# Optimization experiments

Measured on AMD Instinct MI355X. Metric: run time of the kernel, lower is better.

Reference implementation:

```python
import jax, jax.numpy as jnp
import numpy as np

HEADS = 16
DIM_HEAD = 64


def setup_inputs() -> dict:
    key = jax.random.key(0)
    k1, k2, k3, k4, k5 = jax.random.split(key, 5)
    B, S, E = 4, 2048, 1024
    inner = HEADS * DIM_HEAD  # 1024
    return {
        "hidden_states": jax.random.normal(k1, (B, S, E), dtype=jnp.float32),
        "w_q": jax.random.normal(k2, (E, inner), dtype=jnp.float32) * (E ** -0.5),
        "w_k": jax.random.normal(k3, (E, inner), dtype=jnp.float32) * (E ** -0.5),
        "w_v": jax.random.normal(k4, (E, inner), dtype=jnp.float32) * (E ** -0.5),
        "w_o": jax.random.normal(k5, (inner, E), dtype=jnp.float32) * (inner ** -0.5),
    }


def reference(hidden_states, w_q, w_k, w_v, w_o):
    # Self-attention path: context = hidden_states (context arg is None).
    B, S, _ = hidden_states.shape
    dtype = hidden_states.dtype
    scale = DIM_HEAD ** -0.5

    q = (hidden_states @ w_q).reshape(B, S, HEADS, DIM_HEAD)
    k = (hidden_states @ w_k).reshape(B, S, HEADS, DIM_HEAD)
    v = (hidden_states @ w_v).reshape(B, S, HEADS, DIM_HEAD)

    # fp32 softmax as in the original module
    q32 = q.astype(jnp.float32)
    k32 = k.astype(jnp.float32)
    scores = jnp.einsum('btnh,bfnh->bnft', k32, q32) * scale  # [B, H, S_q, S_kv]
    probs = jax.nn.softmax(scores, axis=-1).astype(dtype)

    out = jnp.einsum('bnft,btnh->bfnh', probs, v)  # [B, S, H, D]
    out = out.reshape(B, S, HEADS * DIM_HEAD)
    return out @ w_o  # [B, S, query_dim]
```

## Files before the change

kernel.cpp:

```cpp
#include <hip/hip_runtime.h>
#include <stdint.h>

typedef __attribute__((ext_vector_type(8))) unsigned short ushort8;
typedef __attribute__((ext_vector_type(8))) __bf16 bf16x8;
typedef __attribute__((ext_vector_type(4))) float f32x4;
typedef __attribute__((ext_vector_type(4))) uint32_t u32x4;

#define TBK 32

__device__ __forceinline__ unsigned short f2bf(float f) {
  union { float f; uint32_t u; } x; x.f = f;
  uint32_t u = x.u;
  uint32_t r = (u + 0x7fffu + ((u >> 16) & 1u)) >> 16;
  return (unsigned short)r;
}

__device__ __forceinline__ uint32_t pack_bf2(float lo, float hi) {
  return (uint32_t)f2bf(lo) | ((uint32_t)f2bf(hi) << 16);
}

__device__ __forceinline__ uint32_t rhu2(float lo, float hi) {
  union { float f; uint32_t u; } a, b; a.f = lo; b.f = hi;
  return __builtin_amdgcn_perm(b.u + 0x8000u, a.u + 0x8000u, 0x07060302u);
}

__device__ __forceinline__ void store_c(unsigned short* p, float v) { *p = f2bf(v); }
__device__ __forceinline__ void store_c(float* p, float v) { *p = v; }

__device__ __forceinline__ void gll16(const unsigned short* g, unsigned short* l) {
  __builtin_amdgcn_global_load_lds((const __attribute__((address_space(1))) void*)g,
                                   (__attribute__((address_space(3))) void*)l,
                                   16, 0, 0);
}

__global__ __launch_bounds__(256) void cvt_f32_bf16(
    const float* __restrict__ x, unsigned short* __restrict__ y, int n4) {
  int i = blockIdx.x * 256 + threadIdx.x;
  if (i >= n4) return;
  float4 v = *(const float4*)(x + (size_t)i * 4);
  uint2 p; p.x = pack_bf2(v.x, v.y); p.y = pack_bf2(v.z, v.w);
  *(uint2*)(y + (size_t)i * 4) = p;
}

__global__ void transpose_w(const float* __restrict__ W,
                            unsigned short* __restrict__ WT) {
  __shared__ unsigned short tile[32][33];
  int c0 = blockIdx.x * 32, r0 = blockIdx.y * 32;
  int x = threadIdx.x, y = threadIdx.y;
#pragma unroll
  for (int i = 0; i < 32; i += 8)
    tile[y + i][x] = f2bf(W[(size_t)(r0 + y + i) * 1024 + c0 + x]);
  __syncthreads();
#pragma unroll
  for (int i = 0; i < 32; i += 8)
    WT[(size_t)(c0 + y + i) * 1024 + r0 + x] = tile[x][y + i];
}

template <typename OutT>
__global__ __launch_bounds__(256) void gemm_bt(
    const unsigned short* A,
    const unsigned short* BT0, const unsigned short* BT1, const unsigned short* BT2,
    OutT* C0, OutT* C1, OutT* C2,
    int M, int N, int K, float sc0) {
  const unsigned short* BT = (blockIdx.z == 0) ? BT0 : (blockIdx.z == 1) ? BT1 : BT2;
  OutT* C = (blockIdx.z == 0) ? C0 : (blockIdx.z == 1) ? C1 : C2;
  const float sc = (blockIdx.z == 0) ? sc0 : 1.0f;

  __shared__ __attribute__((aligned(16))) unsigned short As[128 * TBK];
  __shared__ __attribute__((aligned(16))) unsigned short Bs[128 * TBK];

  const int tid = threadIdx.x;
  const int wave = tid >> 6, lane = tid & 63;
  const int fr = lane & 15, fq = lane >> 4;
  const int bm = blockIdx.x * 128, bn = blockIdx.y * 128;
  const int wm = (wave >> 1) * 64, wn = (wave & 1) * 64;

  f32x4 acc[4][4] = {};

  const int sr = lane >> 2;
  const int sk = (lane & 3) * 8;
  const unsigned short* Ag = A + (size_t)(bm + wave * 32 + sr) * K + sk;
  const unsigned short* Bg = BT + (size_t)(bn + wave * 32 + sr) * K + sk;
  unsigned short* As0 = &As[(wave * 32) * TBK];
  unsigned short* Bs0 = &Bs[(wave * 32) * TBK];

  for (int k0 = 0; k0 < K; k0 += TBK) {
    gll16(Ag + k0, As0);
    gll16(Ag + k0 + 16 * K, As0 + 16 * TBK);
    gll16(Bg + k0, Bs0);
    gll16(Bg + k0 + 16 * K, Bs0 + 16 * TBK);
    asm volatile("s_waitcnt vmcnt(0)" ::: "memory");
    __syncthreads();

    bf16x8 af[4], bfr[4];
#pragma unroll
    for (int mt = 0; mt < 4; mt++)
      af[mt] = *(const bf16x8*)&As[(wm + mt * 16 + fr) * TBK + fq * 8];
#pragma unroll
    for (int nt = 0; nt < 4; nt++)
      bfr[nt] = *(const bf16x8*)&Bs[(wn + nt * 16 + fr) * TBK + fq * 8];
#pragma unroll
    for (int mt = 0; mt < 4; mt++)
#pragma unroll
      for (int nt = 0; nt < 4; nt++)
        acc[mt][nt] = __builtin_amdgcn_mfma_f32_16x16x32_bf16(af[mt], bfr[nt], acc[mt][nt], 0, 0, 0);
    __syncthreads();
  }

#pragma unroll
  for (int mt = 0; mt < 4; mt++)
#pragma unroll
    for (int nt = 0; nt < 4; nt++)
#pragma unroll
      for (int r = 0; r < 4; r++) {
        int row = bm + wm + mt * 16 + fq * 4 + r;
        int col = bn + wn + nt * 16 + fr;
        store_c(&C[(size_t)row * N + col], acc[mt][nt][r] * sc);
      }
}

__global__ __launch_bounds__(256, 4) void attn_kernel(
    const unsigned short* q, const unsigned short* k,
    const unsigned short* v, unsigned short* o) {
  const int S = 2048, E = 1024;
  __shared__ __attribute__((aligned(16))) unsigned short Ksb[2 * 64 * 64];
  __shared__ __attribute__((aligned(16))) unsigned short Vtb[64 * 64];

  const int tid = threadIdx.x;
  const int wave = tid >> 6, lane = tid & 63;
  const int fr = lane & 15, fq = lane >> 4;
  const int q0 = blockIdx.x * 128;
  const int bh = blockIdx.y;
  const int b = bh >> 4, h = bh & 15;
  const size_t base = ((size_t)b * S) * E + (size_t)h * 64;

  bf16x8 aq[2][2];
#pragma unroll
  for (int qg = 0; qg < 2; qg++)
#pragma unroll
    for (int ks = 0; ks < 2; ks++)
      aq[qg][ks] = *(const bf16x8*)&q[base +
          (size_t)(q0 + qg * 64 + wave * 16 + fr) * E + ks * 32 + fq * 8];

  ushort8 ones_u;
#pragma unroll
  for (int j = 0; j < 8; j++) ones_u[j] = 0x3F80;
  bf16x8 onesf = *(bf16x8*)&ones_u;

  f32x4 ot[2][4] = {};
  f32x4 osum[2] = {};

  const int srow = lane >> 3;
  const int scol = (((lane & 7) ^ srow) << 3);
  const unsigned short* Kg = k + base + (size_t)(wave * 16 + srow) * E + scol;

  const int rp = (tid & 31) * 2;
  const int dcv = (tid >> 5) * 8;
  const int u_ = rp & 31;
  const int slot = 32 * (rp >> 5) + 8 * ((u_ & 15) >> 2) + 4 * (u_ >> 4) + (u_ & 3);
  const unsigned short* Vg = v + base + (size_t)rp * E + dcv;

  const int rx = (fr & 7) << 3;

  gll16(Kg, &Ksb[wave * 1024]);
  gll16(Kg + 8 * (size_t)E, &Ksb[wave * 1024 + 512]);

  int cur = 0;
  for (int t = 0; t < 32; t++) {
    const int nxt = cur ^ 4096;

    const size_t toff = (size_t)t * 64 * E;
    u32x4 va = *(const u32x4*)(Vg + toff);
    u32x4 vb = *(const u32x4*)(Vg + toff + E);

    __syncthreads();

#pragma unroll
    for (int w = 0; w < 4; w++) {
      uint32_t lo = __builtin_amdgcn_perm(vb[w], va[w], 0x05040100u);
      uint32_t hi = __builtin_amdgcn_perm(vb[w], va[w], 0x07060302u);
      int d = dcv + 2 * w;
      *(uint32_t*)&Vtb[d * 64 + (slot ^ ((2 * w) << 3))] = lo;
      *(uint32_t*)&Vtb[(d + 1) * 64 + (slot ^ ((2 * w + 1) << 3))] = hi;
    }

    __syncthreads();

    if (t < 31) {
      const size_t poff = (size_t)(t + 1) * 64 * E;
      gll16(Kg + poff, &Ksb[nxt + wave * 1024]);
      gll16(Kg + poff + 8 * (size_t)E, &Ksb[nxt + wave * 1024 + 512]);
    }

    f32x4 st[2][4] = {};
    __builtin_amdgcn_s_setprio(1);
#pragma unroll
    for (int ks = 0; ks < 2; ks++) {
#pragma unroll
      for (int tt = 0; tt < 4; tt++) {
        bf16x8 ak = *(const bf16x8*)&Ksb[cur + (tt * 16 + fr) * 64 +
                                         ((ks * 32 + fq * 8) ^ rx)];
        st[0][tt] = __builtin_amdgcn_mfma_f32_16x16x32_bf16(ak, aq[0][ks], st[0][tt], 0, 0, 0);
        st[1][tt] = __builtin_amdgcn_mfma_f32_16x16x32_bf16(ak, aq[1][ks], st[1][tt], 0, 0, 0);
      }
    }
    __builtin_amdgcn_s_setprio(0);

    uint32_t pk[2][4][2];
#pragma unroll
    for (int qg = 0; qg < 2; qg++)
#pragma unroll
      for (int tt = 0; tt < 4; tt++) {
        float e0 = __builtin_amdgcn_exp2f(st[qg][tt][0]);
        float e1 = __builtin_amdgcn_exp2f(st[qg][tt][1]);
        float e2 = __builtin_amdgcn_exp2f(st[qg][tt][2]);
        float e3 = __builtin_amdgcn_exp2f(st[qg][tt][3]);
        pk[qg][tt][0] = rhu2(e0, e1);
        pk[qg][tt][1] = rhu2(e2, e3);
      }

    __builtin_amdgcn_s_setprio(1);
#pragma unroll
    for (int c = 0; c < 2; c++) {
      bf16x8 bp[2];
#pragma unroll
      for (int qg = 0; qg < 2; qg++) {
        u32x4 bpr;
        bpr[0] = pk[qg][2 * c][0];
        bpr[1] = pk[qg][2 * c][1];
        bpr[2] = pk[qg][2 * c + 1][0];
        bpr[3] = pk[qg][2 * c + 1][1];
        bp[qg] = *(bf16x8*)&bpr;
      }
#pragma unroll
      for (int dt = 0; dt < 4; dt++) {
        bf16x8 av = *(const bf16x8*)&Vtb[(dt * 16 + fr) * 64 +
                                         ((c * 32 + fq * 8) ^ rx)];
        ot[0][dt] = __builtin_amdgcn_mfma_f32_16x16x32_bf16(av, bp[0], ot[0][dt], 0, 0, 0);
        ot[1][dt] = __builtin_amdgcn_mfma_f32_16x16x32_bf16(av, bp[1], ot[1][dt], 0, 0, 0);
      }
      osum[0] = __builtin_amdgcn_mfma_f32_16x16x32_bf16(onesf, bp[0], osum[0], 0, 0, 0);
      osum[1] = __builtin_amdgcn_mfma_f32_16x16x32_bf16(onesf, bp[1], osum[1], 0, 0, 0);
    }
    __builtin_amdgcn_s_setprio(0);

    cur = nxt;
  }

#pragma unroll
  for (int qg = 0; qg < 2; qg++) {
    float inv = 1.0f / osum[qg][0];
    size_t rowbase = base + (size_t)(q0 + qg * 64 + wave * 16 + fr) * E;
#pragma unroll
    for (int dt = 0; dt < 4; dt++) {
      uint32_t w0 = rhu2(ot[qg][dt][0] * inv, ot[qg][dt][1] * inv);
      uint32_t w1 = rhu2(ot[qg][dt][2] * inv, ot[qg][dt][3] * inv);
      *(uint32_t*)&o[rowbase + dt * 16 + fq * 4] = w0;
      *(uint32_t*)&o[rowbase + dt * 16 + fq * 4 + 2] = w1;
    }
  }
}

extern "C" void kernel_launch(void* const* d_in, const int* in_sizes, int n_in,
                              void* d_out, int out_size, void* d_ws, size_t ws_size,
                              hipStream_t stream) {
  const float* hs = (const float*)d_in[0];
  const float* wq = (const float*)d_in[1];
  const float* wk = (const float*)d_in[2];
  const float* wv = (const float*)d_in[3];
  const float* wo = (const float*)d_in[4];
  unsigned short* ws = (unsigned short*)d_ws;

  unsigned short* wqT = ws;
  unsigned short* wkT = ws + 1048576;
  unsigned short* wvT = ws + 2097152;
  unsigned short* woT = wqT;
  unsigned short* qb  = ws + 3145728;
  unsigned short* kb  = qb + 8388608;
  unsigned short* vb  = kb + 8388608;
  unsigned short* ob  = qb;
  unsigned short* hsb = (unsigned short*)d_out;
  float* out = (float*)d_out;

  const int M = 8192, N = 1024, K = 1024;
  const float KSC = 0.125f * 1.44269504088896341f;

  cvt_f32_bf16<<<dim3(M * K / 4 / 256), 256, 0, stream>>>(hs, hsb, M * K / 4);

  dim3 tb(32, 8);
  transpose_w<<<dim3(32, 32), tb, 0, stream>>>(wq, wqT);
  transpose_w<<<dim3(32, 32), tb, 0, stream>>>(wk, wkT);
  transpose_w<<<dim3(32, 32), tb, 0, stream>>>(wv, wvT);

  gemm_bt<unsigned short><<<dim3(M / 128, N / 128, 3), 256, 0, stream>>>(
      hsb, wqT, wkT, wvT, qb, kb, vb, M, N, K, KSC);

  transpose_w<<<dim3(32, 32), tb, 0, stream>>>(wo, woT);

  attn_kernel<<<dim3(2048 / 128, 64), 256, 0, stream>>>(qb, kb, vb, ob);

  gemm_bt<float><<<dim3(M / 128, N / 128, 1), 256, 0, stream>>>(
      ob, woT, woT, woT, out, out, out, M, N, K, 1.0f);
}
```

Before: 279.1 us.

## Double-buffer GEMM with 128x256 tiles, BK=64, XOR-swizzled LDS, fused transposes

Rewrites the projection GEMM to use 512-thread blocks computing 128x256 tiles. K steps are now 64 wide, and the next tile is prefetched into a second LDS buffer with global_load_lds while MFMAs run on the current one. The LDS column chunks are XOR-swizzled so fragment reads avoid bank conflicts. The three weight transposes are also merged into one launch. The goal is to hide global-load latency, halve the barriers per K element and cut launch count, at the price of more LDS (96KB per block) and fewer resident blocks.

```diff
diff --git a/kernel.cpp b/kernel.cpp
--- a/kernel.cpp
+++ b/kernel.cpp
@@ -5,8 +5,6 @@
 typedef __attribute__((ext_vector_type(8))) __bf16 bf16x8;
 typedef __attribute__((ext_vector_type(4))) float f32x4;
 typedef __attribute__((ext_vector_type(4))) uint32_t u32x4;
-
-#define TBK 32
 
 __device__ __forceinline__ unsigned short f2bf(float f) {
   union { float f; uint32_t u; } x; x.f = f;
@@ -42,8 +40,7 @@
   *(uint2*)(y + (size_t)i * 4) = p;
 }
 
-__global__ void transpose_w(const float* __restrict__ W,
-                            unsigned short* __restrict__ WT) {
+__device__ __forceinline__ void transpose_body(const float* W, unsigned short* WT) {
   __shared__ unsigned short tile[32][33];
   int c0 = blockIdx.x * 32, r0 = blockIdx.y * 32;
   int x = threadIdx.x, y = threadIdx.y;
@@ -56,8 +53,21 @@
     WT[(size_t)(c0 + y + i) * 1024 + r0 + x] = tile[x][y + i];
 }
 
+__global__ void transpose_w(const float* __restrict__ W,
+                            unsigned short* __restrict__ WT) {
+  transpose_body(W, WT);
+}
+
+__global__ void transpose_w3(const float* W0, const float* W1, const float* W2,
+                             unsigned short* T0, unsigned short* T1,
+                             unsigned short* T2) {
+  const float* W = (blockIdx.z == 0) ? W0 : (blockIdx.z == 1) ? W1 : W2;
+  unsigned short* WT = (blockIdx.z == 0) ? T0 : (blockIdx.z == 1) ? T1 : T2;
+  transpose_body(W, WT);
+}
+
 template <typename OutT>
-__global__ __launch_bounds__(256) void gemm_bt(
+__global__ __launch_bounds__(512, 2) void gemm2(
     const unsigned short* A,
     const unsigned short* BT0, const unsigned short* BT1, const unsigned short* BT2,
     OutT* C0, OutT* C1, OutT* C2,
@@ -66,55 +76,77 @@
   OutT* C = (blockIdx.z == 0) ? C0 : (blockIdx.z == 1) ? C1 : C2;
   const float sc = (blockIdx.z == 0) ? sc0 : 1.0f;
 
-  __shared__ __attribute__((aligned(16))) unsigned short As[128 * TBK];
-  __shared__ __attribute__((aligned(16))) unsigned short Bs[128 * TBK];
+  __shared__ __attribute__((aligned(16))) unsigned short As[2][128 * 64];
+  __shared__ __attribute__((aligned(16))) unsigned short Bs[2][256 * 64];
 
   const int tid = threadIdx.x;
   const int wave = tid >> 6, lane = tid & 63;
   const int fr = lane & 15, fq = lane >> 4;
-  const int bm = blockIdx.x * 128, bn = blockIdx.y * 128;
-  const int wm = (wave >> 1) * 64, wn = (wave & 1) * 64;
+  const int wm = wave >> 2, wn = wave & 3;
+  const int bm = blockIdx.x * 128, bn = blockIdx.y * 256;
+
+  const int r8 = tid >> 3, c8 = tid & 7;
+  const int s8 = c8 ^ (r8 & 7);
+  const unsigned short* Ag = A + (size_t)(bm + r8) * K + s8 * 8;
+  const unsigned short* Bg = BT + (size_t)(bn + r8) * K + s8 * 8;
 
   f32x4 acc[4][4] = {};
-
-  const int sr = lane >> 2;
-  const int sk = (lane & 3) * 8;
-  const unsigned short* Ag = A + (size_t)(bm + wave * 32 + sr) * K + sk;
-  const unsigned short* Bg = BT + (size_t)(bn + wave * 32 + sr) * K + sk;
-  unsigned short* As0 = &As[(wave * 32) * TBK];
-  unsigned short* Bs0 = &Bs[(wave * 32) * TBK];
-
-  for (int k0 = 0; k0 < K; k0 += TBK) {
-    gll16(Ag + k0, As0);
-    gll16(Ag + k0 + 16 * K, As0 + 16 * TBK);
-    gll16(Bg + k0, Bs0);
-    gll16(Bg + k0 + 16 * K, Bs0 + 16 * TBK);
-    asm volatile("s_waitcnt vmcnt(0)" ::: "memory");
+  const int rx = fr & 7;
+
+  const int NT = K >> 6;
+
+  {
+    gll16(Ag, &As[0][(wave * 8) * 64]);
+    gll16(Ag + 64 * (size_t)K, &As[0][(64 + wave * 8) * 64]);
+    gll16(Bg, &Bs[0][(wave * 8) * 64]);
+    gll16(Bg + 64 * (size_t)K, &Bs[0][(64 + wave * 8) * 64]);
+    gll16(Bg + 128 * (size_t)K, &Bs[0][(128 + wave * 8) * 64]);
+    gll16(Bg + 192 * (size_t)K, &Bs[0][(192 + wave * 8) * 64]);
+  }
+
+  int cur = 0;
+  for (int t = 0; t < NT; ++t) {
     __syncthreads();
 
-    bf16x8 af[4], bfr[4];
-#pragma unroll
-    for (int mt = 0; mt < 4; mt++)
-      af[mt] = *(const bf16x8*)&As[(wm + mt * 16 + fr) * TBK + fq * 8];
+    if (t + 1 < NT) {
+      const int b = cur ^ 1;
+      const size_t k0 = (size_t)(t + 1) * 64;
+      gll16(Ag + k0, &As[b][(wave * 8) * 64]);
+      gll16(Ag + k0 + 64 * (size_t)K, &As[b][(64 + wave * 8) * 64]);
+      gll16(Bg + k0, &Bs[b][(wave * 8) * 64]);
+      gll16(Bg + k0 + 64 * (size_t)K, &Bs[b][(64 + wave * 8) * 64]);
+      gll16(Bg + k0 + 128 * (size_t)K, &Bs[b][(128 + wave * 8) * 64]);
+      gll16(Bg + k0 + 192 * (size_t)K, &Bs[b][(192 + wave * 8) * 64]);
+    }
+
+#pragma unroll
+    for (int kh = 0; kh < 2; ++kh) {
+      bf16x8 af[4], bfr[4];
+#pragma unroll
+      for (int mt = 0; mt < 4; mt++)
+        af[mt] = *(const bf16x8*)&As[cur][(wm * 64 + mt * 16 + fr) * 64 +
+                                          (((kh * 4 + fq) ^ rx) * 8)];
+#pragma unroll
+      for (int nt = 0; nt < 4; nt++)
+        bfr[nt] = *(const bf16x8*)&Bs[cur][(wn * 64 + nt * 16 + fr) * 64 +
+                                           (((kh * 4 + fq) ^ rx) * 8)];
+#pragma unroll
+      for (int mt = 0; mt < 4; mt++)
+#pragma unroll
+        for (int nt = 0; nt < 4; nt++)
+          acc[mt][nt] = __builtin_amdgcn_mfma_f32_16x16x32_bf16(af[mt], bfr[nt], acc[mt][nt], 0, 0, 0);
+    }
+    cur ^= 1;
+  }
+
+#pragma unroll
+  for (int mt = 0; mt < 4; mt++)
 #pragma unroll
     for (int nt = 0; nt < 4; nt++)
-      bfr[nt] = *(const bf16x8*)&Bs[(wn + nt * 16 + fr) * TBK + fq * 8];
-#pragma unroll
-    for (int mt = 0; mt < 4; mt++)
-#pragma unroll
-      for (int nt = 0; nt < 4; nt++)
-        acc[mt][nt] = __builtin_amdgcn_mfma_f32_16x16x32_bf16(af[mt], bfr[nt], acc[mt][nt], 0, 0, 0);
-    __syncthreads();
-  }
-
-#pragma unroll
-  for (int mt = 0; mt < 4; mt++)
-#pragma unroll
-    for (int nt = 0; nt < 4; nt++)
 #pragma unroll
       for (int r = 0; r < 4; r++) {
-        int row = bm + wm + mt * 16 + fq * 4 + r;
-        int col = bn + wn + nt * 16 + fr;
+        int row = bm + wm * 64 + mt * 16 + fq * 4 + r;
+        int col = bn + wn * 64 + nt * 16 + fr;
         store_c(&C[(size_t)row * N + col], acc[mt][nt][r] * sc);
       }
 }
@@ -288,17 +320,15 @@
   cvt_f32_bf16<<<dim3(M * K / 4 / 256), 256, 0, stream>>>(hs, hsb, M * K / 4);
 
   dim3 tb(32, 8);
-  transpose_w<<<dim3(32, 32), tb, 0, stream>>>(wq, wqT);
-  transpose_w<<<dim3(32, 32), tb, 0, stream>>>(wk, wkT);
-  transpose_w<<<dim3(32, 32), tb, 0, stream>>>(wv, wvT);
-
-  gemm_bt<unsigned short><<<dim3(M / 128, N / 128, 3), 256, 0, stream>>>(
+  transpose_w3<<<dim3(32, 32, 3), tb, 0, stream>>>(wq, wk, wv, wqT, wkT, wvT);
+
+  gemm2<unsigned short><<<dim3(M / 128, N / 256, 3), 512, 0, stream>>>(
       hsb, wqT, wkT, wvT, qb, kb, vb, M, N, K, KSC);
 
   transpose_w<<<dim3(32, 32), tb, 0, stream>>>(wo, woT);
 
   attn_kernel<<<dim3(2048 / 128, 64), 256, 0, stream>>>(qb, kb, vb, ob);
 
-  gemm_bt<float><<<dim3(M / 128, N / 128, 1), 256, 0, stream>>>(
+  gemm2<float><<<dim3(M / 128, N / 256, 1), 512, 0, stream>>>(
       ob, woT, woT, woT, out, out, out, M, N, K, 1.0f);
 }
```

After: 276.2 us. Within noise of the previous version (-1.0%).
